# Kernel tuning notes

Measured on AMD Instinct MI355X. Metric: run time of the kernel, lower is better.

Reference implementation:

```python
import jax, jax.numpy as jnp
import numpy as np

N_NODES = 100000
N_EDGES = 1600000
DIMS = [100, 200, 128, 128]
EPS = 1e-5


def setup_inputs() -> dict:
    key = jax.random.key(0)
    ks = jax.random.split(key, 32)
    inp = {
        "x": jax.random.normal(ks[0], (N_NODES, DIMS[0]), dtype=jnp.float32),
        "edge_row": jnp.sort(jax.random.randint(ks[1], (N_EDGES,), 0, N_NODES, dtype=jnp.int32)),
        "edge_col": jax.random.randint(ks[2], (N_EDGES,), 0, N_NODES, dtype=jnp.int32),
        "edge_val": jax.random.uniform(ks[3], (N_EDGES,), dtype=jnp.float32),
    }
    # GCwithself layer params: neighbor-agg linear W,b and self linear Ws,bs
    ki = 4
    for i in range(3):
        fi, fo = DIMS[i], DIMS[i + 1]
        s = 1.0 / np.sqrt(fi)
        inp[f"gc{i}_W"] = jax.random.uniform(ks[ki], (fi, fo), minval=-s, maxval=s); ki += 1
        inp[f"gc{i}_b"] = jnp.zeros((fo,), jnp.float32)
        inp[f"gc{i}_Ws"] = jax.random.uniform(ks[ki], (fi, fo), minval=-s, maxval=s); ki += 1
        inp[f"gc{i}_bs"] = jnp.zeros((fo,), jnp.float32)
    s = 1.0 / np.sqrt(128)
    inp["fc1_W"] = jax.random.uniform(ks[ki], (128, 128), minval=-s, maxval=s); ki += 1
    inp["fc1_b"] = jnp.zeros((128,), jnp.float32)
    inp["fc2a_W"] = jax.random.uniform(ks[ki], (128, 256), minval=-s, maxval=s); ki += 1
    inp["fc2a_b"] = jnp.zeros((256,), jnp.float32)
    inp["bn_g"] = jnp.ones((256,), jnp.float32)
    inp["bn_b"] = jnp.zeros((256,), jnp.float32)
    s2 = 1.0 / np.sqrt(256)
    inp["fc2b_W"] = jax.random.uniform(ks[ki], (256, 18), minval=-s2, maxval=s2); ki += 1
    inp["fc2b_b"] = jnp.zeros((18,), jnp.float32)
    return inp


def _gc_layer(x, row, col, val, W, b, Ws, bs):
    # spmm: (adj @ x) via gather + segment-sum, then linear + self-linear + ReLU
    agg = jax.ops.segment_sum(val[:, None] * x[col], row, num_segments=N_NODES)
    return jax.nn.relu(agg @ W + b + x @ Ws + bs)


def _batchnorm(h, g, b):
    mu = jnp.mean(h, axis=0)
    var = jnp.var(h, axis=0)
    return (h - mu) * jax.lax.rsqrt(var + EPS) * g + b


def reference(x, edge_row, edge_col, edge_val,
              gc0_W, gc0_b, gc0_Ws, gc0_bs,
              gc1_W, gc1_b, gc1_Ws, gc1_bs,
              gc2_W, gc2_b, gc2_Ws, gc2_bs,
              fc1_W, fc1_b, fc2a_W, fc2a_b, bn_g, bn_b, fc2b_W, fc2b_b):
    h = _gc_layer(x, edge_row, edge_col, edge_val, gc0_W, gc0_b, gc0_Ws, gc0_bs)
    h = _gc_layer(h, edge_row, edge_col, edge_val, gc1_W, gc1_b, gc1_Ws, gc1_bs)
    h = _gc_layer(h, edge_row, edge_col, edge_val, gc2_W, gc2_b, gc2_Ws, gc2_bs)
    h = jax.nn.relu(h @ fc1_W + fc1_b)
    h = _batchnorm(h @ fc2a_W + fc2a_b, bn_g, bn_b)
    h = jax.nn.relu(h)
    return h @ fc2b_W + fc2b_b
```

## Files before the change

kernel.cpp:

```cpp
#include <hip/hip_runtime.h>

#define N_NODES 100000
#define N_EDGES 1600000
#define NTILE64 1563
#define LDP 1568

#define MEMFENCE asm volatile("" ::: "memory")

typedef __attribute__((ext_vector_type(8))) short bf16x8;
typedef __attribute__((ext_vector_type(4))) float f32x4;

__device__ __forceinline__ unsigned short f2bf(float f) {
    unsigned u = __float_as_uint(f);
    u = (u + 0x7FFFu + ((u >> 16) & 1u)) >> 16;
    return (unsigned short)u;
}
__device__ __forceinline__ float bf2f(unsigned short h) {
    return __uint_as_float(((unsigned)h) << 16);
}
__device__ __forceinline__ float bflo(unsigned w) { return __uint_as_float(w << 16); }
__device__ __forceinline__ float bfhi(unsigned w) { return __uint_as_float(w & 0xFFFF0000u); }

__device__ __forceinline__ bf16x8 ld_frag(const unsigned short* p) {
    return *(const bf16x8*)p;
}

__global__ void build_row_ptr(const int* __restrict__ row, int* __restrict__ rp) {
    int n = blockIdx.x * blockDim.x + threadIdx.x;
    if (n > N_NODES) return;
    int lo = 0, hi = N_EDGES;
    while (lo < hi) {
        int mid = (lo + hi) >> 1;
        if (row[mid] < n) lo = mid + 1; else hi = mid;
    }
    rp[n] = lo;
}

__global__ __launch_bounds__(256) void conv_x(const float* __restrict__ x,
                                              unsigned short* __restrict__ xb) {
    const int total = N_NODES * 104;
    for (int i = blockIdx.x * 256 + threadIdx.x; i < total; i += gridDim.x * 256) {
        int r = i / 104, c = i - r * 104;
        xb[i] = (c < 100) ? f2bf(x[(size_t)r * 100 + c]) : (unsigned short)0;
    }
}

__global__ __launch_bounds__(256) void prep_all(
    const float* __restrict__ gc0W, const float* __restrict__ gc0Ws,
    const float* __restrict__ gc1W, const float* __restrict__ gc1Ws,
    const float* __restrict__ gc2W, const float* __restrict__ gc2Ws,
    const float* __restrict__ f1W,  const float* __restrict__ f2aW,
    const float* __restrict__ f2bW,
    const float* __restrict__ gc0b, const float* __restrict__ gc0bs,
    const float* __restrict__ gc2b, const float* __restrict__ gc2bs,
    const float* __restrict__ gc1b, const float* __restrict__ gc1bs,
    unsigned short* __restrict__ Bt0, unsigned short* __restrict__ Bt1,
    unsigned short* __restrict__ Bt2, unsigned short* __restrict__ Btf1,
    unsigned short* __restrict__ Btf2a, unsigned short* __restrict__ Btf2b,
    float* __restrict__ bias0, float* __restrict__ bias2, float* __restrict__ bias1)
{
    int i = blockIdx.x * 256 + threadIdx.x;
    if (i < 44800) {
        int n = i / 224, k = i - n * 224; float v = 0.f;
        if (k < 104) { if (k < 100) v = gc0W[(size_t)k * 200 + n]; }
        else { int kr = k - 104; if (kr < 100) v = gc0Ws[(size_t)kr * 200 + n]; }
        Bt0[i] = f2bf(v); return;
    }
    i -= 44800;
    if (i < 57344) {
        int n = i / 224, k = i - n * 224; float v = 0.f;
        if (k < 200) v = (n < 128) ? gc1W[(size_t)k * 128 + n] : gc1Ws[(size_t)k * 128 + (n - 128)];
        Bt1[i] = f2bf(v); return;
    }
    i -= 57344;
    if (i < 32768) {
        int n = i / 256, k = i - n * 256; float v;
        if (k < 128) v = gc2W[(size_t)k * 128 + n];
        else         v = gc2Ws[(size_t)(k - 128) * 128 + n];
        Bt2[i] = f2bf(v); return;
    }
    i -= 32768;
    if (i < 16384) { int n = i >> 7, k = i & 127; Btf1[i] = f2bf(f1W[(size_t)k * 128 + n]); return; }
    i -= 16384;
    if (i < 32768) { int n = i >> 7, k = i & 127; Btf2a[i] = f2bf(f2aW[(size_t)k * 256 + n]); return; }
    i -= 32768;
    if (i < 4608) { int n = i >> 8, k = i & 255; Btf2b[i] = f2bf(f2bW[(size_t)k * 18 + n]); return; }
    i -= 4608;
    if (i < 200) { bias0[i] = gc0b[i] + gc0bs[i]; return; }
    i -= 200;
    if (i < 128) { bias2[i] = gc2b[i] + gc2bs[i]; return; }
    i -= 128;
    if (i < 128) { bias1[i] = gc1b[i] + gc1bs[i]; return; }
}

template<int FUSE>
__global__ __launch_bounds__(256) void spmm_v4(
    const unsigned short* __restrict__ xin, int ldin, int F,
    const int* __restrict__ rp, const int* __restrict__ col,
    const float* __restrict__ val, const float* __restrict__ b01,
    unsigned short* __restrict__ outp, int ldout)
{
    const int node = blockIdx.x * 16 + (threadIdx.x >> 4);
    const int l16 = threadIdx.x & 15;
    const int f8 = l16 * 8;
    const bool act = f8 < F;
    const int e0 = rp[node], e1 = rp[node + 1];
    const unsigned short* xf = xin + f8;

    float a[8];
#pragma unroll
    for (int k = 0; k < 8; k++) a[k] = 0.f;

    for (int e = e0; e < e1; e += 4) {
        int   cj[4]; float vj[4];
#pragma unroll
        for (int j = 0; j < 4; j++) {
            int ej = e + j;
            bool m = ej < e1;
            int es = m ? ej : e0;
            cj[j] = col[es];
            float vv = val[es];
            vj[j] = m ? vv : 0.f;
        }
        if (act) {
#pragma unroll
            for (int j = 0; j < 4; j++) {
                uint4 u = *(const uint4*)(xf + (size_t)cj[j] * ldin);
                float v = vj[j];
                a[0] += v * bflo(u.x); a[1] += v * bfhi(u.x);
                a[2] += v * bflo(u.y); a[3] += v * bfhi(u.y);
                a[4] += v * bflo(u.z); a[5] += v * bfhi(u.z);
                a[6] += v * bflo(u.w); a[7] += v * bfhi(u.w);
            }
        }
    }

    if (act) {
        if (FUSE) {
            uint4 uz = *(const uint4*)(xin + (size_t)node * ldin + 128 + f8);
            float z[8] = {bflo(uz.x), bfhi(uz.x), bflo(uz.y), bfhi(uz.y),
                          bflo(uz.z), bfhi(uz.z), bflo(uz.w), bfhi(uz.w)};
#pragma unroll
            for (int k = 0; k < 8; k++)
                a[k] = fmaxf(a[k] + z[k] + b01[f8 + k], 0.f);
        }
        uint4 pk;
        pk.x = ((unsigned)f2bf(a[1]) << 16) | (unsigned)f2bf(a[0]);
        pk.y = ((unsigned)f2bf(a[3]) << 16) | (unsigned)f2bf(a[2]);
        pk.z = ((unsigned)f2bf(a[5]) << 16) | (unsigned)f2bf(a[4]);
        pk.w = ((unsigned)f2bf(a[7]) << 16) | (unsigned)f2bf(a[6]);
        *(uint4*)(outp + (size_t)node * ldout + f8) = pk;
    }
}

__global__ __launch_bounds__(256) void gemm_head(
    const unsigned short* __restrict__ agg0, const unsigned short* __restrict__ xb,
    const unsigned short* __restrict__ Bt0, const float* __restrict__ bias0,
    const unsigned short* __restrict__ Bt1,
    unsigned short* __restrict__ yz, int M)
{
    __shared__ __align__(16) unsigned short H[64][264];

    const int tid = threadIdx.x;
    const int rowBase = blockIdx.x * 64;
    const int wave = tid >> 6, lane = tid & 63;
    const int cb = wave * 64;
    const int lrow = lane & 15, lq = lane >> 4;
    const int kq = lq * 8;

    {
        f32x4 acc[4][4] = {};
        for (int kk = 0; kk < 224; kk += 32) {
            int k0 = kk + kq;
            bf16x8 af[4], bfr[4];
#pragma unroll
            for (int m = 0; m < 4; ++m) {
                int gr = rowBase + 16 * m + lrow;
                bf16x8 t = {};
                if (gr < M && k0 < 208)
                    t = (k0 < 104) ? ld_frag(agg0 + (size_t)gr * 104 + k0)
                                   : ld_frag(xb   + (size_t)gr * 104 + (k0 - 104));
                af[m] = t;
            }
#pragma unroll
            for (int n = 0; n < 4; ++n) {
                int nr = cb + 16 * n + lrow;
                bf16x8 t = {};
                if (nr < 200) t = ld_frag(Bt0 + (size_t)nr * 224 + k0);
                bfr[n] = t;
            }
#pragma unroll
            for (int m = 0; m < 4; ++m)
#pragma unroll
                for (int n = 0; n < 4; ++n)
                    acc[m][n] = __builtin_amdgcn_mfma_f32_16x16x32_bf16(af[m], bfr[n], acc[m][n], 0, 0, 0);
        }
#pragma unroll
        for (int n = 0; n < 4; ++n) {
            int colg = cb + 16 * n + lrow;
            if (colg >= 224) continue;
            float bb = (colg < 200) ? bias0[colg] : 0.f;
#pragma unroll
            for (int m = 0; m < 4; ++m)
#pragma unroll
                for (int r = 0; r < 4; ++r) {
                    int rowl = 16 * m + lq * 4 + r;
                    H[rowl][colg] = f2bf(fmaxf(acc[m][n][r] + bb, 0.f));
                }
        }
    }
    __syncthreads();

    {
        f32x4 acc[4][4] = {};
        for (int kk = 0; kk < 224; kk += 32) {
            int k0 = kk + kq;
            bf16x8 af[4], bfr[4];
#pragma unroll
            for (int m = 0; m < 4; ++m) af[m] = *(const bf16x8*)&H[16 * m + lrow][k0];
#pragma unroll
            for (int n = 0; n < 4; ++n)
                bfr[n] = ld_frag(Bt1 + (size_t)(cb + 16 * n + lrow) * 224 + k0);
#pragma unroll
            for (int m = 0; m < 4; ++m)
#pragma unroll
                for (int n = 0; n < 4; ++n)
                    acc[m][n] = __builtin_amdgcn_mfma_f32_16x16x32_bf16(af[m], bfr[n], acc[m][n], 0, 0, 0);
        }
        __syncthreads();
#pragma unroll
        for (int n = 0; n < 4; ++n) {
            int colg = cb + 16 * n + lrow;
#pragma unroll
            for (int m = 0; m < 4; ++m)
#pragma unroll
                for (int r = 0; r < 4; ++r) {
                    int rowl = 16 * m + lq * 4 + r;
                    H[rowl][colg] = f2bf(acc[m][n][r]);
                }
        }
    }
    __syncthreads();
#pragma unroll
    for (int i = 0; i < 8; ++i) {
        int c = tid + 256 * i;
        int row = c >> 5;
        int ch  = c & 31;
        int rowg = rowBase + row;
        if (rowg < M)
            *(uint4*)(yz + (size_t)rowg * 256 + ch * 8) = *(const uint4*)&H[row][ch * 8];
    }
}

__global__ __launch_bounds__(256) void gemm_tail(
    const unsigned short* __restrict__ agg2, const unsigned short* __restrict__ h1,
    const unsigned short* __restrict__ Bt2, const float* __restrict__ bias2,
    const unsigned short* __restrict__ Btf1, const float* __restrict__ fc1b,
    const unsigned short* __restrict__ Btf2a, const float* __restrict__ fc2ab,
    unsigned short* __restrict__ h4, float* __restrict__ P, int M)
{
    __shared__ __align__(16) unsigned short H[64][264];

    const int tid = threadIdx.x;
    const int rowBase = blockIdx.x * 64;
    const int wave = tid >> 6, lane = tid & 63;
    const int lrow = lane & 15, lq = lane >> 4;
    const int kq = lq * 8;

    {
        const int cb = wave * 32;
        f32x4 acc[4][2] = {};
        bf16x8 Bf[8][2];
#pragma unroll
        for (int ki = 0; ki < 8; ++ki)
#pragma unroll
            for (int n = 0; n < 2; ++n)
                Bf[ki][n] = ld_frag(Bt2 + (size_t)(cb + 16 * n + lrow) * 256 + 32 * ki + kq);
        MEMFENCE;
        bf16x8 A2[2][4];
#pragma unroll
        for (int m = 0; m < 4; ++m) {
            int gr = rowBase + 16 * m + lrow;
            bf16x8 t = {};
            if (gr < M) t = ld_frag(agg2 + (size_t)gr * 128 + kq);
            A2[0][m] = t;
        }
        MEMFENCE;
#pragma unroll
        for (int ki = 0; ki < 8; ++ki) {
            const int cur = ki & 1;
            if (ki < 7) {
                const int kin = ki + 1;
                int k0 = 32 * kin + kq;
                const unsigned short* Asrc = (kin < 4) ? agg2 : h1;
                int krel = (kin < 4) ? k0 : k0 - 128;
#pragma unroll
                for (int m = 0; m < 4; ++m) {
                    int gr = rowBase + 16 * m + lrow;
                    bf16x8 t = {};
                    if (gr < M) t = ld_frag(Asrc + (size_t)gr * 128 + krel);
                    A2[cur ^ 1][m] = t;
                }
            }
            MEMFENCE;
#pragma unroll
            for (int m = 0; m < 4; ++m)
#pragma unroll
                for (int n = 0; n < 2; ++n)
                    acc[m][n] = __builtin_amdgcn_mfma_f32_16x16x32_bf16(A2[cur][m], Bf[ki][n], acc[m][n], 0, 0, 0);
        }
#pragma unroll
        for (int n = 0; n < 2; ++n) {
            int colg = cb + 16 * n + lrow;
            float bb = bias2[colg];
#pragma unroll
            for (int m = 0; m < 4; ++m)
#pragma unroll
                for (int r = 0; r < 4; ++r) {
                    int rowl = 16 * m + lq * 4 + r;
                    H[rowl][colg] = f2bf(fmaxf(acc[m][n][r] + bb, 0.f));
                }
        }
    }
    __syncthreads();

    {
        const int cb = wave * 32;
        f32x4 acc[4][2] = {};
        bf16x8 Bf[4][2];
#pragma unroll
        for (int ki = 0; ki < 4; ++ki)
#pragma unroll
            for (int n = 0; n < 2; ++n)
                Bf[ki][n] = ld_frag(Btf1 + (size_t)(cb + 16 * n + lrow) * 128 + 32 * ki + kq);
        MEMFENCE;
#pragma unroll
        for (int ki = 0; ki < 4; ++ki) {
            bf16x8 af[4];
#pragma unroll
            for (int m = 0; m < 4; ++m) af[m] = *(const bf16x8*)&H[16 * m + lrow][32 * ki + kq];
#pragma unroll
            for (int m = 0; m < 4; ++m)
#pragma unroll
                for (int n = 0; n < 2; ++n)
                    acc[m][n] = __builtin_amdgcn_mfma_f32_16x16x32_bf16(af[m], Bf[ki][n], acc[m][n], 0, 0, 0);
        }
        __syncthreads();
#pragma unroll
        for (int n = 0; n < 2; ++n) {
            int colg = cb + 16 * n + lrow;
            float bb = fc1b[colg];
#pragma unroll
            for (int m = 0; m < 4; ++m)
#pragma unroll
                for (int r = 0; r < 4; ++r) {
                    int rowl = 16 * m + lq * 4 + r;
                    H[rowl][colg] = f2bf(fmaxf(acc[m][n][r] + bb, 0.f));
                }
        }
    }
    __syncthreads();

    {
        const int cb = wave * 64;
        f32x4 acc[4][4] = {};
        bf16x8 Bf[4][4];
#pragma unroll
        for (int ki = 0; ki < 4; ++ki)
#pragma unroll
            for (int n = 0; n < 4; ++n)
                Bf[ki][n] = ld_frag(Btf2a + (size_t)(cb + 16 * n + lrow) * 128 + 32 * ki + kq);
        MEMFENCE;
#pragma unroll
        for (int ki = 0; ki < 4; ++ki) {
            bf16x8 af[4];
#pragma unroll
            for (int m = 0; m < 4; ++m) af[m] = *(const bf16x8*)&H[16 * m + lrow][32 * ki + kq];
#pragma unroll
            for (int m = 0; m < 4; ++m)
#pragma unroll
                for (int n = 0; n < 4; ++n)
                    acc[m][n] = __builtin_amdgcn_mfma_f32_16x16x32_bf16(af[m], Bf[ki][n], acc[m][n], 0, 0, 0);
        }
        __syncthreads();

#pragma unroll
        for (int n = 0; n < 4; ++n) {
            int colg = cb + 16 * n + lrow;
            float bb = fc2ab[colg];
            float s = 0.f, s2 = 0.f;
#pragma unroll
            for (int m = 0; m < 4; ++m)
#pragma unroll
                for (int r = 0; r < 4; ++r) {
                    int rowl = 16 * m + lq * 4 + r;
                    float v = acc[m][n][r] + bb;
                    H[rowl][colg] = f2bf(v);
                    if (rowBase + rowl < M) { s += v; s2 += v * v; }
                }
            s  += __shfl_xor(s, 16);  s  += __shfl_xor(s, 32);
            s2 += __shfl_xor(s2, 16); s2 += __shfl_xor(s2, 32);
            if (lq == 0) {
                P[(size_t)colg * LDP + blockIdx.x] = s;
                P[(size_t)(256 + colg) * LDP + blockIdx.x] = s2;
            }
        }
        __syncthreads();
#pragma unroll
        for (int i = 0; i < 8; ++i) {
            int c = tid + 256 * i;
            int row = c >> 5;
            int ch  = c & 31;
            int rowg = rowBase + row;
            if (rowg < M)
                *(uint4*)(h4 + (size_t)rowg * 256 + ch * 8) = *(const uint4*)&H[row][ch * 8];
        }
    }
}

__global__ __launch_bounds__(256) void bn_reduce(const float* __restrict__ P,
                                                 const float* __restrict__ g,
                                                 const float* __restrict__ b,
                                                 float* __restrict__ stats) {
    const int c = blockIdx.x;
    const int tid = threadIdx.x;
    __shared__ float r1[256], r2[256];
    float s = 0.f, s2 = 0.f;
    for (int i = tid; i < NTILE64; i += 256) {
        s  += P[(size_t)c * LDP + i];
        s2 += P[(size_t)(256 + c) * LDP + i];
    }
    r1[tid] = s; r2[tid] = s2;
    __syncthreads();
    for (int off = 128; off > 0; off >>= 1) {
        if (tid < off) { r1[tid] += r1[tid + off]; r2[tid] += r2[tid + off]; }
        __syncthreads();
    }
    if (tid == 0) {
        const float invN = 1.f / (float)N_NODES;
        float mu = r1[0] * invN;
        float var = r2[0] * invN - mu * mu;
        float sc = g[c] * rsqrtf(var + 1e-5f);
        stats[512 + c] = sc;
        stats[768 + c] = b[c] - mu * sc;
    }
}

__global__ __launch_bounds__(256) void fc2b_kernel(
    const unsigned short* __restrict__ h4, const unsigned short* __restrict__ Btf2b,
    const float* __restrict__ bias, const float* __restrict__ stats,
    float* __restrict__ out, int M)
{
    const int tid = threadIdx.x;
    const int wave = tid >> 6, lane = tid & 63;
    const int lrow = lane & 15, lq = lane >> 4;
    const int kq = lq * 8;
    const int rowBase = blockIdx.x * 128 + wave * 32;

    f32x4 acc[2][2] = {};
    for (int kk = 0; kk < 256; kk += 32) {
        int k0 = kk + kq;
        const float* sc = stats + 512 + k0;
        const float* sh = stats + 768 + k0;
        bf16x8 af[2], bfr[2];
#pragma unroll
        for (int m = 0; m < 2; ++m) {
            int gr = rowBase + 16 * m + lrow;
            uint4 u = make_uint4(0, 0, 0, 0);
            if (gr < M) u = *(const uint4*)(h4 + (size_t)gr * 256 + k0);
            unsigned w[4] = {u.x, u.y, u.z, u.w};
#pragma unroll
            for (int j = 0; j < 4; j++) {
                float lo = fmaxf(bflo(w[j]) * sc[2 * j] + sh[2 * j], 0.f);
                float hi = fmaxf(bfhi(w[j]) * sc[2 * j + 1] + sh[2 * j + 1], 0.f);
                w[j] = ((unsigned)f2bf(hi) << 16) | (unsigned)f2bf(lo);
            }
            uint4 packed = make_uint4(w[0], w[1], w[2], w[3]);
            af[m] = *(const bf16x8*)&packed;
        }
#pragma unroll
        for (int n = 0; n < 2; ++n) {
            int nr = 16 * n + lrow;
            bf16x8 t = {};
            if (nr < 18) t = ld_frag(Btf2b + (size_t)nr * 256 + k0);
            bfr[n] = t;
        }
#pragma unroll
        for (int m = 0; m < 2; ++m)
#pragma unroll
            for (int n = 0; n < 2; ++n)
                acc[m][n] = __builtin_amdgcn_mfma_f32_16x16x32_bf16(af[m], bfr[n], acc[m][n], 0, 0, 0);
    }
#pragma unroll
    for (int n = 0; n < 2; ++n) {
        int colg = 16 * n + lrow;
        if (colg >= 18) continue;
        float bb = bias[colg];
#pragma unroll
        for (int m = 0; m < 2; ++m)
#pragma unroll
            for (int r = 0; r < 4; ++r) {
                int rowg = rowBase + 16 * m + lq * 4 + r;
                if (rowg < M)
                    out[(size_t)rowg * 18 + colg] = acc[m][n][r] + bb;
            }
    }
}

extern "C" void kernel_launch(void* const* d_in, const int* in_sizes, int n_in,
                              void* d_out, int out_size, void* d_ws, size_t ws_size,
                              hipStream_t stream) {
    const float* x        = (const float*)d_in[0];
    const int*   edge_row = (const int*)  d_in[1];
    const int*   edge_col = (const int*)  d_in[2];
    const float* edge_val = (const float*)d_in[3];
    const float* gc0_W  = (const float*)d_in[4];
    const float* gc0_b  = (const float*)d_in[5];
    const float* gc0_Ws = (const float*)d_in[6];
    const float* gc0_bs = (const float*)d_in[7];
    const float* gc1_W  = (const float*)d_in[8];
    const float* gc1_b  = (const float*)d_in[9];
    const float* gc1_Ws = (const float*)d_in[10];
    const float* gc1_bs = (const float*)d_in[11];
    const float* gc2_W  = (const float*)d_in[12];
    const float* gc2_b  = (const float*)d_in[13];
    const float* gc2_Ws = (const float*)d_in[14];
    const float* gc2_bs = (const float*)d_in[15];
    const float* fc1_W  = (const float*)d_in[16];
    const float* fc1_b  = (const float*)d_in[17];
    const float* fc2a_W = (const float*)d_in[18];
    const float* fc2a_b = (const float*)d_in[19];
    const float* bn_g   = (const float*)d_in[20];
    const float* bn_b   = (const float*)d_in[21];
    const float* fc2b_W = (const float*)d_in[22];
    const float* fc2b_b = (const float*)d_in[23];
    float* out = (float*)d_out;

    char* ws = (char*)d_ws;
    int*   rowptr = (int*)ws;
    float* stats  = (float*)(ws + 512 * 1024);
    size_t o = 520 * 1024;
    unsigned short* Bt0   = (unsigned short*)(ws + o); o += 200 * 224 * 2;
    unsigned short* Bt1   = (unsigned short*)(ws + o); o += 256 * 224 * 2;
    unsigned short* Bt2   = (unsigned short*)(ws + o); o += 128 * 256 * 2;
    unsigned short* Btf1  = (unsigned short*)(ws + o); o += 128 * 128 * 2;
    unsigned short* Btf2a = (unsigned short*)(ws + o); o += 256 * 128 * 2;
    unsigned short* Btf2b = (unsigned short*)(ws + o); o += 18 * 256 * 2;
    float* bias0 = (float*)(ws + o); o += 200 * 4;
    float* bias2 = (float*)(ws + o); o += 128 * 4;
    float* bias1 = (float*)(ws + o); o += 128 * 4;
    const size_t SLOT = 52u * 1024 * 1024;
    char* S1 = ws + 1 * 1024 * 1024;
    char* S2 = S1 + SLOT;
    char* S3 = S2 + SLOT;

    unsigned short* xb   = (unsigned short*)S1;
    unsigned short* agg0 = (unsigned short*)S2;
    unsigned short* yz   = (unsigned short*)S3;
    unsigned short* h1   = (unsigned short*)S1;
    unsigned short* agg2 = (unsigned short*)S2;
    unsigned short* h4   = (unsigned short*)S3;
    float* Pp = (float*)(S2 + 40u * 1024 * 1024);

    build_row_ptr<<<392, 256, 0, stream>>>(edge_row, rowptr);
    conv_x<<<2048, 256, 0, stream>>>(x, xb);
    prep_all<<<(189128 + 255) / 256, 256, 0, stream>>>(
        gc0_W, gc0_Ws, gc1_W, gc1_Ws, gc2_W, gc2_Ws, fc1_W, fc2a_W, fc2b_W,
        gc0_b, gc0_bs, gc2_b, gc2_bs, gc1_b, gc1_bs,
        Bt0, Bt1, Bt2, Btf1, Btf2a, Btf2b, bias0, bias2, bias1);

    const int spmmGrid = N_NODES / 16;

    spmm_v4<0><<<spmmGrid, 256, 0, stream>>>(xb, 104, 104, rowptr, edge_col, edge_val,
                                             nullptr, agg0, 104);
    gemm_head<<<NTILE64, 256, 0, stream>>>(agg0, xb, Bt0, bias0, Bt1, yz, N_NODES);
    spmm_v4<1><<<spmmGrid, 256, 0, stream>>>(yz, 256, 128, rowptr, edge_col, edge_val,
                                             bias1, h1, 128);
    spmm_v4<0><<<spmmGrid, 256, 0, stream>>>(h1, 128, 128, rowptr, edge_col, edge_val,
                                             nullptr, agg2, 128);
    gemm_tail<<<NTILE64, 256, 0, stream>>>(
        agg2, h1, Bt2, bias2, Btf1, fc1_b, Btf2a, fc2a_b, h4, Pp, N_NODES);
    bn_reduce<<<256, 256, 0, stream>>>(Pp, bn_g, bn_b, stats);
    fc2b_kernel<<<(N_NODES + 127) / 128, 256, 0, stream>>>(
        h4, Btf2b, fc2b_b, stats, out, N_NODES);
}
```

Before: 490.0 us.

## Split SpMM feature columns across XCDs and pad input features to 128

The SpMM kernel is reorganised so that blockIdx&7 picks a 16-column feature slice. Blocks are dispatched round-robin across the 8 XCDs, so each XCD's L2 caches only its slice of the gathered feature matrix, which is meant to raise the L2 hit rate on the random gathers. Each thread pair now handles 16 features of one node, and the main loop issues all four gathers before accumulating. The input features are padded from 104 to 128 columns (with matching changes to Bt0 and gemm_head) so every slice is full, at the cost of extra padded traffic and compute. The BN partial-sum buffer is also transposed to a row-major per-block layout.

```diff
diff --git a/kernel.cpp b/kernel.cpp
--- a/kernel.cpp
+++ b/kernel.cpp
@@ -3,7 +3,6 @@
 #define N_NODES 100000
 #define N_EDGES 1600000
 #define NTILE64 1563
-#define LDP 1568
 
 #define MEMFENCE asm volatile("" ::: "memory")
 
@@ -38,9 +37,9 @@
 
 __global__ __launch_bounds__(256) void conv_x(const float* __restrict__ x,
                                               unsigned short* __restrict__ xb) {
-    const int total = N_NODES * 104;
+    const int total = N_NODES * 128;
     for (int i = blockIdx.x * 256 + threadIdx.x; i < total; i += gridDim.x * 256) {
-        int r = i / 104, c = i - r * 104;
+        int r = i >> 7, c = i & 127;
         xb[i] = (c < 100) ? f2bf(x[(size_t)r * 100 + c]) : (unsigned short)0;
     }
 }
@@ -60,13 +59,13 @@
     float* __restrict__ bias0, float* __restrict__ bias2, float* __restrict__ bias1)
 {
     int i = blockIdx.x * 256 + threadIdx.x;
-    if (i < 44800) {
-        int n = i / 224, k = i - n * 224; float v = 0.f;
-        if (k < 104) { if (k < 100) v = gc0W[(size_t)k * 200 + n]; }
-        else { int kr = k - 104; if (kr < 100) v = gc0Ws[(size_t)kr * 200 + n]; }
+    if (i < 51200) {
+        int n = i >> 8, k = i & 255; float v = 0.f;
+        if (k < 128) { if (k < 100) v = gc0W[(size_t)k * 200 + n]; }
+        else { int kr = k - 128; if (kr < 100) v = gc0Ws[(size_t)kr * 200 + n]; }
         Bt0[i] = f2bf(v); return;
     }
-    i -= 44800;
+    i -= 51200;
     if (i < 57344) {
         int n = i / 224, k = i - n * 224; float v = 0.f;
         if (k < 200) v = (n < 128) ? gc1W[(size_t)k * 128 + n] : gc1Ws[(size_t)k * 128 + (n - 128)];
@@ -94,63 +93,63 @@
 }
 
 template<int FUSE>
-__global__ __launch_bounds__(256) void spmm_v4(
-    const unsigned short* __restrict__ xin, int ldin, int F,
+__global__ __launch_bounds__(256) void spmm_xcd(
+    const unsigned short* __restrict__ xin, int ldin,
     const int* __restrict__ rp, const int* __restrict__ col,
     const float* __restrict__ val, const float* __restrict__ b01,
     unsigned short* __restrict__ outp, int ldout)
 {
-    const int node = blockIdx.x * 16 + (threadIdx.x >> 4);
-    const int l16 = threadIdx.x & 15;
-    const int f8 = l16 * 8;
-    const bool act = f8 < F;
+    const int slice = blockIdx.x & 7;
+    const int node  = (blockIdx.x >> 3) * 128 + (threadIdx.x >> 1);
+    if (node >= N_NODES) return;
+    const int fbase = slice * 16 + (threadIdx.x & 1) * 8;
     const int e0 = rp[node], e1 = rp[node + 1];
-    const unsigned short* xf = xin + f8;
+    const unsigned short* xf = xin + fbase;
 
     float a[8];
 #pragma unroll
     for (int k = 0; k < 8; k++) a[k] = 0.f;
 
-    for (int e = e0; e < e1; e += 4) {
-        int   cj[4]; float vj[4];
+    int e = e0;
+    for (; e + 4 <= e1; e += 4) {
+        int   cj[4]; float vj[4]; uint4 u[4];
+#pragma unroll
+        for (int j = 0; j < 4; j++) { cj[j] = col[e + j]; vj[j] = val[e + j]; }
+#pragma unroll
+        for (int j = 0; j < 4; j++)
+            u[j] = *(const uint4*)(xf + (size_t)cj[j] * ldin);
 #pragma unroll
         for (int j = 0; j < 4; j++) {
-            int ej = e + j;
-            bool m = ej < e1;
-            int es = m ? ej : e0;
-            cj[j] = col[es];
-            float vv = val[es];
-            vj[j] = m ? vv : 0.f;
-        }
-        if (act) {
-#pragma unroll
-            for (int j = 0; j < 4; j++) {
-                uint4 u = *(const uint4*)(xf + (size_t)cj[j] * ldin);
-                float v = vj[j];
-                a[0] += v * bflo(u.x); a[1] += v * bfhi(u.x);
-                a[2] += v * bflo(u.y); a[3] += v * bfhi(u.y);
-                a[4] += v * bflo(u.z); a[5] += v * bfhi(u.z);
-                a[6] += v * bflo(u.w); a[7] += v * bfhi(u.w);
-            }
-        }
-    }
-
-    if (act) {
-        if (FUSE) {
-            uint4 uz = *(const uint4*)(xin + (size_t)node * ldin + 128 + f8);
-            float z[8] = {bflo(uz.x), bfhi(uz.x), bflo(uz.y), bfhi(uz.y),
-                          bflo(uz.z), bfhi(uz.z), bflo(uz.w), bfhi(uz.w)};
-#pragma unroll
-            for (int k = 0; k < 8; k++)
-                a[k] = fmaxf(a[k] + z[k] + b01[f8 + k], 0.f);
-        }
-        uint4 pk;
-        pk.x = ((unsigned)f2bf(a[1]) << 16) | (unsigned)f2bf(a[0]);
-        pk.y = ((unsigned)f2bf(a[3]) << 16) | (unsigned)f2bf(a[2]);
-        pk.z = ((unsigned)f2bf(a[5]) << 16) | (unsigned)f2bf(a[4]);
-        pk.w = ((unsigned)f2bf(a[7]) << 16) | (unsigned)f2bf(a[6]);
-        *(uint4*)(outp + (size_t)node * ldout + f8) = pk;
-    }
+            float v = vj[j];
+            a[0] += v * bflo(u[j].x); a[1] += v * bfhi(u[j].x);
+            a[2] += v * bflo(u[j].y); a[3] += v * bfhi(u[j].y);
+            a[4] += v * bflo(u[j].z); a[5] += v * bfhi(u[j].z);
+            a[6] += v * bflo(u[j].w); a[7] += v * bfhi(u[j].w);
+        }
+    }
+    for (; e < e1; ++e) {
+        int c0 = col[e]; float v0 = val[e];
+        uint4 u0 = *(const uint4*)(xf + (size_t)c0 * ldin);
+        a[0] += v0 * bflo(u0.x); a[1] += v0 * bfhi(u0.x);
+        a[2] += v0 * bflo(u0.y); a[3] += v0 * bfhi(u0.y);
+        a[4] += v0 * bflo(u0.z); a[5] += v0 * bfhi(u0.z);
+        a[6] += v0 * bflo(u0.w); a[7] += v0 * bfhi(u0.w);
+    }
+
+    if (FUSE) {
+        uint4 uz = *(const uint4*)(xin + (size_t)node * ldin + 128 + fbase);
+        float z[8] = {bflo(uz.x), bfhi(uz.x), bflo(uz.y), bfhi(uz.y),
+                      bflo(uz.z), bfhi(uz.z), bflo(uz.w), bfhi(uz.w)};
+#pragma unroll
+        for (int k = 0; k < 8; k++)
+            a[k] = fmaxf(a[k] + z[k] + b01[fbase + k], 0.f);
+    }
+    uint4 pk;
+    pk.x = ((unsigned)f2bf(a[1]) << 16) | (unsigned)f2bf(a[0]);
+    pk.y = ((unsigned)f2bf(a[3]) << 16) | (unsigned)f2bf(a[2]);
+    pk.z = ((unsigned)f2bf(a[5]) << 16) | (unsigned)f2bf(a[4]);
+    pk.w = ((unsigned)f2bf(a[7]) << 16) | (unsigned)f2bf(a[6]);
+    *(uint4*)(outp + (size_t)node * ldout + fbase) = pk;
 }
 
 __global__ __launch_bounds__(256) void gemm_head(
@@ -170,23 +169,23 @@
 
     {
         f32x4 acc[4][4] = {};
-        for (int kk = 0; kk < 224; kk += 32) {
+        for (int kk = 0; kk < 256; kk += 32) {
             int k0 = kk + kq;
             bf16x8 af[4], bfr[4];
 #pragma unroll
             for (int m = 0; m < 4; ++m) {
                 int gr = rowBase + 16 * m + lrow;
                 bf16x8 t = {};
-                if (gr < M && k0 < 208)
-                    t = (k0 < 104) ? ld_frag(agg0 + (size_t)gr * 104 + k0)
-                                   : ld_frag(xb   + (size_t)gr * 104 + (k0 - 104));
+                if (gr < M)
+                    t = (k0 < 128) ? ld_frag(agg0 + (size_t)gr * 128 + k0)
+                                   : ld_frag(xb   + (size_t)gr * 128 + (k0 - 128));
                 af[m] = t;
             }
 #pragma unroll
             for (int n = 0; n < 4; ++n) {
                 int nr = cb + 16 * n + lrow;
                 bf16x8 t = {};
-                if (nr < 200) t = ld_frag(Bt0 + (size_t)nr * 224 + k0);
+                if (nr < 200) t = ld_frag(Bt0 + (size_t)nr * 256 + k0);
                 bfr[n] = t;
             }
 #pragma unroll
@@ -401,8 +400,8 @@
             s  += __shfl_xor(s, 16);  s  += __shfl_xor(s, 32);
             s2 += __shfl_xor(s2, 16); s2 += __shfl_xor(s2, 32);
             if (lq == 0) {
-                P[(size_t)colg * LDP + blockIdx.x] = s;
-                P[(size_t)(256 + colg) * LDP + blockIdx.x] = s2;
+                P[(size_t)blockIdx.x * 512 + colg] = s;
+                P[(size_t)blockIdx.x * 512 + 256 + colg] = s2;
             }
         }
         __syncthreads();
@@ -427,8 +426,8 @@
     __shared__ float r1[256], r2[256];
     float s = 0.f, s2 = 0.f;
     for (int i = tid; i < NTILE64; i += 256) {
-        s  += P[(size_t)c * LDP + i];
-        s2 += P[(size_t)(256 + c) * LDP + i];
+        s  += P[(size_t)i * 512 + c];
+        s2 += P[(size_t)i * 512 + 256 + c];
     }
     r1[tid] = s; r2[tid] = s2;
     __syncthreads();
@@ -540,7 +539,7 @@
     int*   rowptr = (int*)ws;
     float* stats  = (float*)(ws + 512 * 1024);
     size_t o = 520 * 1024;
-    unsigned short* Bt0   = (unsigned short*)(ws + o); o += 200 * 224 * 2;
+    unsigned short* Bt0   = (unsigned short*)(ws + o); o += 200 * 256 * 2;
     unsigned short* Bt1   = (unsigned short*)(ws + o); o += 256 * 224 * 2;
     unsigned short* Bt2   = (unsigned short*)(ws + o); o += 128 * 256 * 2;
     unsigned short* Btf1  = (unsigned short*)(ws + o); o += 128 * 128 * 2;
@@ -564,20 +563,20 @@
 
     build_row_ptr<<<392, 256, 0, stream>>>(edge_row, rowptr);
     conv_x<<<2048, 256, 0, stream>>>(x, xb);
-    prep_all<<<(189128 + 255) / 256, 256, 0, stream>>>(
+    prep_all<<<(195528 + 255) / 256, 256, 0, stream>>>(
         gc0_W, gc0_Ws, gc1_W, gc1_Ws, gc2_W, gc2_Ws, fc1_W, fc2a_W, fc2b_W,
         gc0_b, gc0_bs, gc2_b, gc2_bs, gc1_b, gc1_bs,
         Bt0, Bt1, Bt2, Btf1, Btf2a, Btf2b, bias0, bias2, bias1);
 
-    const int spmmGrid = N_NODES / 16;
-
-    spmm_v4<0><<<spmmGrid, 256, 0, stream>>>(xb, 104, 104, rowptr, edge_col, edge_val,
-                                             nullptr, agg0, 104);
+    const int spmmGrid = 782 * 8;
+
+    spmm_xcd<0><<<spmmGrid, 256, 0, stream>>>(xb, 128, rowptr, edge_col, edge_val,
+                                              nullptr, agg0, 128);
     gemm_head<<<NTILE64, 256, 0, stream>>>(agg0, xb, Bt0, bias0, Bt1, yz, N_NODES);
-    spmm_v4<1><<<spmmGrid, 256, 0, stream>>>(yz, 256, 128, rowptr, edge_col, edge_val,
-                                             bias1, h1, 128);
-    spmm_v4<0><<<spmmGrid, 256, 0, stream>>>(h1, 128, 128, rowptr, edge_col, edge_val,
-                                             nullptr, agg2, 128);
+    spmm_xcd<1><<<spmmGrid, 256, 0, stream>>>(yz, 256, rowptr, edge_col, edge_val,
+                                              bias1, h1, 128);
+    spmm_xcd<0><<<spmmGrid, 256, 0, stream>>>(h1, 128, rowptr, edge_col, edge_val,
+                                              nullptr, agg2, 128);
     gemm_tail<<<NTILE64, 256, 0, stream>>>(
         agg2, h1, Bt2, bias2, Btf1, fc1_b, Btf2a, fc2a_b, h4, Pp, N_NODES);
     bn_reduce<<<256, 256, 0, stream>>>(Pp, bn_g, bn_b, stats);
```

Result: slower. 1.126 ms (+129.8%).
